# Kernel optimization log

Measured on AMD Instinct MI355X. Metric: run time of the kernel, lower is better.

## Reference

```python
import jax, jax.numpy as jnp
import numpy as np

THETA = 128.0


def _make_Q(d, units):
    # Q[n,m] = (2n+1)/sqrt(d) if n > m and (n+m) odd, else 0 (fixed, non-trainable)
    n = np.arange(d)[:, None]
    m = np.arange(units)[None, :]
    Q = np.where((n > m) & (((n + m) % 2) == 1), (2 * n + 1) / np.sqrt(d), 0.0)
    return jnp.asarray(Q, dtype=jnp.float32)


def setup_inputs() -> dict:
    key = jax.random.key(0)
    k1, k2, k3, k4 = jax.random.split(key, 4)
    B_, T, Din, d, units = 16, 4096, 128, 256, 256
    x = jax.random.normal(k1, (B_, T, Din), dtype=jnp.float32)
    A = jax.random.normal(k2, (d, d), dtype=jnp.float32) / np.sqrt(d)
    Bm = jax.random.normal(k3, (Din, d), dtype=jnp.float32) / np.sqrt(Din)
    W_mix = jax.random.normal(k4, (units, units), dtype=jnp.float32) / np.sqrt(units)
    b_mix = jnp.zeros((units,), dtype=jnp.float32)
    return {"x": x, "A": A, "B": Bm, "W_mix": W_mix, "b_mix": b_mix}


def reference(x, A, B, W_mix, b_mix):
    d = A.shape[0]
    units = W_mix.shape[0]
    Q = _make_Q(d, units)
    QW = Q @ W_mix  # fuse fixed projection with dense kernel: (d, units)
    alpha = 1.0 - 1.0 / THETA
    beta = 1.0 / THETA
    # precompute input projection for all steps: (T, batch, d)
    xB = jnp.einsum('bti,id->tbd', x, B)

    def step(state, xBt):
        new_state = alpha * state + beta * (state @ A + xBt)
        y = jnp.tanh(new_state @ QW + b_mix)
        return new_state, y

    s0 = jnp.zeros((x.shape[0], d), dtype=x.dtype)
    _, ys = jax.lax.scan(step, s0, xB)  # ys: (T, batch, units)
    return jnp.transpose(ys, (1, 0, 2))
```

## Files before the change

kernel.cpp:

```cpp
#include <hip/hip_runtime.h>
#include <math.h>

constexpr int T_   = 4096;
constexpr int NB   = 16;
constexpr int D_   = 256;
constexpr int DIN  = 128;
constexpr int U_   = 256;
constexpr int L1   = 8;
constexpr int C1   = T_ / L1;
constexpr float ALPHA_ = 1.0f - 1.0f / 128.0f;
constexpr float BETA_  = 1.0f / 128.0f;
constexpr int SD   = NB * D_;
constexpr int MS   = D_ * D_;
constexpr int TLP  = D_ + 4;
constexpr int XLP  = DIN + 4;

using short8  = __attribute__((ext_vector_type(8))) short;
using float4v = __attribute__((ext_vector_type(4))) float;

__device__ __forceinline__ unsigned short bf16_rne(float x) {
  const unsigned b = __float_as_uint(x);
  const unsigned r = ((b >> 16) & 1u) + 0x7FFFu;
  return (unsigned short)((b + r) >> 16);
}
__device__ __forceinline__ float bf16_f(unsigned short h) {
  return __uint_as_float(((unsigned)h) << 16);
}

__device__ __forceinline__ void split2(float e0, float e1, unsigned& hd, unsigned& ld) {
  const unsigned b0 = __float_as_uint(e0), b1 = __float_as_uint(e1);
  const unsigned h0 = b0 & 0xFFFF0000u, h1 = b1 & 0xFFFF0000u;
  const float l0 = e0 - __uint_as_float(h0);
  const float l1 = e1 - __uint_as_float(h1);
  hd = (h0 >> 16) | h1;
  ld = (__float_as_uint(l0) >> 16) | (__float_as_uint(l1) & 0xFFFF0000u);
}

__device__ __forceinline__ void unpack8(uint4 a, uint4 b, short8& hi, short8& lo) {
  union { short8 s; unsigned u[4]; } H, L;
  const unsigned d[8] = {a.x, a.y, a.z, a.w, b.x, b.y, b.z, b.w};
#pragma unroll
  for (int i = 0; i < 4; ++i) {
    H.u[i] = (d[2 * i] >> 16) | (d[2 * i + 1] & 0xFFFF0000u);
    L.u[i] = (d[2 * i] & 0xFFFFu) | (d[2 * i + 1] << 16);
  }
  hi = H.s; lo = L.s;
}

__device__ __forceinline__ int nwpar(int c, int l) {
  if (c <= 0) return 0;
  const int f = 31 - __clz(c);
  const int nw = (l < f + 1) ? l : (f + 1);
  return nw & 1;
}

__device__ __forceinline__ void mm_row(const float* __restrict__ Am,
                                       const float* __restrict__ Bm,
                                       float* __restrict__ Dm,
                                       int i, int tid, float* srow) {
  srow[tid] = Am[i * D_ + tid];
  __syncthreads();
  float a0 = 0.f, a1 = 0.f, a2 = 0.f, a3 = 0.f;
#pragma unroll 8
  for (int k = 0; k < D_; k += 4) {
    a0 = fmaf(srow[k + 0], Bm[(k + 0) * D_ + tid], a0);
    a1 = fmaf(srow[k + 1], Bm[(k + 1) * D_ + tid], a1);
    a2 = fmaf(srow[k + 2], Bm[(k + 2) * D_ + tid], a2);
    a3 = fmaf(srow[k + 3], Bm[(k + 3) * D_ + tid], a3);
  }
  Dm[i * D_ + tid] = (a0 + a1) + (a2 + a3);
  __syncthreads();
}

__global__ __launch_bounds__(256) void k_prep(const float* __restrict__ A,
                                              const float* __restrict__ W,
                                              float* __restrict__ Meff,
                                              float* __restrict__ QW,
                                              const float* __restrict__ Bm,
                                              unsigned short* __restrict__ Mf,
                                              unsigned short* __restrict__ Bmf) {
  const int bid = blockIdx.x, tid = threadIdx.x;
  if (bid < D_) {
    float v = BETA_ * A[bid * D_ + tid];
    if (bid == tid) v += ALPHA_;
    Meff[bid * D_ + tid] = v;
    return;
  }
  if (bid == D_) {
    __shared__ float wch[32 * D_];
    float se = 0.f, so = 0.f;
    for (int ch = 0; ch < D_ / 32; ++ch) {
      __syncthreads();
      for (int idx = tid; idx < 32 * D_; idx += 256)
        wch[idx] = W[ch * 32 * D_ + idx];
      __syncthreads();
#pragma unroll
      for (int r = 0; r < 32; ++r) {
        const int n = ch * 32 + r;
        const float sum = (n & 1) ? se : so;
        QW[n * U_ + tid] = sum * ((float)(2 * n + 1) / 16.0f);
        const float wv = wch[r * D_ + tid];
        if (n & 1) so += wv; else se += wv;
      }
    }
    return;
  }
  const int pb = bid - D_ - 1;
  const int lane = tid & 63, nb0 = tid >> 6;
  const int quad = lane >> 4, m16 = lane & 15;
  if (pb < 8) {
    const int ks = pb;
    for (int nb = nb0; nb < 16; nb += 4) {
      const size_t fo = ((size_t)(nb * 8 + ks) * 64 + lane) * 8;
#pragma unroll
      for (int jj = 0; jj < 8; ++jj) {
        const int k = ks * 32 + quad * 8 + jj;
        const int n = nb * 16 + m16;
        const float v = BETA_ * A[k * D_ + n];
        const unsigned short h = bf16_rne(v);
        Mf[fo + jj] = h;
        Mf[MS + fo + jj] = bf16_rne(v - bf16_f(h));
      }
    }
  } else {
    const int ks = pb - 8;
    unsigned short* dh = Bmf;
    unsigned short* dl = Bmf + (MS / 2);
    for (int nb = nb0; nb < 16; nb += 4) {
      const size_t fo = ((size_t)(nb * 4 + ks) * 64 + lane) * 8;
#pragma unroll
      for (int jj = 0; jj < 8; ++jj) {
        const int k = ks * 32 + quad * 8 + jj;
        const int n = nb * 16 + m16;
        const float v = BETA_ * Bm[k * D_ + n];
        const unsigned short h = bf16_rne(v);
        dh[fo + jj] = h;
        dl[fo + jj] = bf16_rne(v - bf16_f(h));
      }
    }
  }
}

__global__ __launch_bounds__(256) void k_pw(const float* __restrict__ Am,
                                            const float* __restrict__ Bbase,
                                            float* __restrict__ Dbase) {
  __shared__ float srow[D_];
  const int q = blockIdx.x >> 8, row = blockIdx.x & 255;
  mm_row(Am, Bbase + (size_t)q * MS, Dbase + (size_t)q * MS, row, threadIdx.x, srow);
}

__global__ __launch_bounds__(256) void k_pwr(const float* __restrict__ Abase,
                                             const float* __restrict__ Bm,
                                             float* __restrict__ Dbase) {
  __shared__ float srow[D_];
  const int q = blockIdx.x >> 8, row = blockIdx.x & 255;
  mm_row(Abase + (size_t)q * MS, Bm, Dbase + (size_t)q * MS, row, threadIdx.x, srow);
}

__global__ __launch_bounds__(256, 2) void k_big2(
    const float* __restrict__ R, const float* __restrict__ QWm,
    const float* __restrict__ M8, unsigned short* __restrict__ Bf,
    unsigned short* __restrict__ Pf0,
    const float* __restrict__ x, const unsigned short* __restrict__ Bmf,
    const unsigned short* __restrict__ Mf,
    unsigned short* __restrict__ Shi, unsigned short* __restrict__ Slo,
    float* __restrict__ Ends) {
  const int bid = blockIdx.x, tid = threadIdx.x;
  if (bid < 80) {
    const int mat = bid >> 3, ks = bid & 7;
    const float* X = (mat < 8) ? (R + (size_t)mat * MS) : (mat == 8 ? QWm : M8);
    unsigned short* dh = (mat < 9) ? (Bf + (size_t)mat * (2 * MS)) : Pf0;
    unsigned short* dl = dh + MS;
    const int lane = tid & 63, nb0 = tid >> 6;
    const int quad = lane >> 4, m16 = lane & 15;
    for (int nb = nb0; nb < 16; nb += 4) {
      const size_t fo = ((size_t)(nb * 8 + ks) * 64 + lane) * 8;
#pragma unroll
      for (int jj = 0; jj < 8; ++jj) {
        const int k = ks * 32 + quad * 8 + jj;
        const int n = nb * 16 + m16;
        const float xv = X[k * D_ + n];
        const unsigned short h = bf16_rne(xv);
        dh[fo + jj] = h;
        dl[fo + jj] = bf16_rne(xv - bf16_f(h));
      }
    }
    return;
  }
  __shared__ __align__(16) float xls[NB][XLP];
  __shared__ __align__(16) unsigned tls[NB][TLP];
  const int c = bid - 80;
  const int w = tid >> 6, lane = tid & 63;
  const int m16 = lane & 15, q = lane >> 4;
  const int xrow = tid >> 4, xi0 = (tid & 15) * 8;

  float4v sC[4];
#pragma unroll
  for (int nt = 0; nt < 4; ++nt) sC[nt] = (float4v){0.f, 0.f, 0.f, 0.f};

  for (int j = 0; j < L1; ++j) {
    const int t = c * L1 + j;
    __syncthreads();
    {
      const float* xr = x + ((size_t)xrow * T_ + t) * DIN + xi0;
      const float4 v0 = *(const float4*)(xr);
      const float4 v1 = *(const float4*)(xr + 4);
      *(float4*)(&xls[xrow][xi0]) = v0;
      *(float4*)(&xls[xrow][xi0 + 4]) = v1;
    }
    if (j > 0) {
#pragma unroll
      for (int nt = 0; nt < 4; ++nt) {
        const int n = (w * 4 + nt) * 16 + m16;
#pragma unroll
        for (int r = 0; r < 4; ++r) {
          const float sv = sC[nt][r];
          const unsigned hb = __float_as_uint(sv) & 0xFFFF0000u;
          const float lo = sv - __uint_as_float(hb);
          tls[4 * q + r][n] = hb | (__float_as_uint(lo) >> 16);
        }
      }
    }
    __syncthreads();
    float4v acc[4];
#pragma unroll
    for (int nt = 0; nt < 4; ++nt) {
      acc[nt][0] = ALPHA_ * sC[nt][0];
      acc[nt][1] = ALPHA_ * sC[nt][1];
      acc[nt][2] = ALPHA_ * sC[nt][2];
      acc[nt][3] = ALPHA_ * sC[nt][3];
    }
#pragma unroll
    for (int ks = 0; ks < 4; ++ks) {
      float xv[8];
      *(float4*)(xv)     = *(const float4*)(&xls[m16][32 * ks + 8 * q]);
      *(float4*)(xv + 4) = *(const float4*)(&xls[m16][32 * ks + 8 * q + 4]);
      union { short8 s; unsigned u[4]; } XH, XL;
#pragma unroll
      for (int p = 0; p < 4; ++p) split2(xv[2 * p], xv[2 * p + 1], XH.u[p], XL.u[p]);
#pragma unroll
      for (int nt = 0; nt < 4; ++nt) {
        const size_t fo = ((size_t)((w * 4 + nt) * 4 + ks) * 64 + lane) * 8;
        const short8 bh = *(const short8*)(Bmf + fo);
        const short8 bl = *(const short8*)(Bmf + (MS / 2) + fo);
        acc[nt] = __builtin_amdgcn_mfma_f32_16x16x32_bf16(XH.s, bh, acc[nt], 0, 0, 0);
        acc[nt] = __builtin_amdgcn_mfma_f32_16x16x32_bf16(XH.s, bl, acc[nt], 0, 0, 0);
        acc[nt] = __builtin_amdgcn_mfma_f32_16x16x32_bf16(XL.s, bh, acc[nt], 0, 0, 0);
      }
    }
    if (j > 0) {
#pragma unroll
      for (int ks = 0; ks < 8; ++ks) {
        const uint4 p0 = *(const uint4*)(&tls[m16][32 * ks + 8 * q]);
        const uint4 p1 = *(const uint4*)(&tls[m16][32 * ks + 8 * q + 4]);
        short8 sh, sl; unpack8(p0, p1, sh, sl);
        if ((ks & 3) == w) {
          const size_t ao = ((size_t)((t - 1) * 8 + ks) * 64 + lane) * 8;
          *(short8*)(Shi + ao) = sh;
          *(short8*)(Slo + ao) = sl;
        }
#pragma unroll
        for (int nt = 0; nt < 4; ++nt) {
          const size_t fo = ((size_t)((w * 4 + nt) * 8 + ks) * 64 + lane) * 8;
          const short8 mh = *(const short8*)(Mf + fo);
          const short8 ml = *(const short8*)(Mf + MS + fo);
          acc[nt] = __builtin_amdgcn_mfma_f32_16x16x32_bf16(sh, mh, acc[nt], 0, 0, 0);
          acc[nt] = __builtin_amdgcn_mfma_f32_16x16x32_bf16(sh, ml, acc[nt], 0, 0, 0);
          acc[nt] = __builtin_amdgcn_mfma_f32_16x16x32_bf16(sl, mh, acc[nt], 0, 0, 0);
        }
      }
    }
#pragma unroll
    for (int nt = 0; nt < 4; ++nt) sC[nt] = acc[nt];
  }
  const int tl = c * L1 + L1 - 1;
  __syncthreads();
#pragma unroll
  for (int nt = 0; nt < 4; ++nt) {
    const int n = (w * 4 + nt) * 16 + m16;
#pragma unroll
    for (int r = 0; r < 4; ++r) {
      const float sv = sC[nt][r];
      const unsigned hb = __float_as_uint(sv) & 0xFFFF0000u;
      const float lo = sv - __uint_as_float(hb);
      tls[4 * q + r][n] = hb | (__float_as_uint(lo) >> 16);
    }
  }
  __syncthreads();
#pragma unroll
  for (int kk = 0; kk < 2; ++kk) {
    const int ks = w + kk * 4;
    const uint4 p0 = *(const uint4*)(&tls[m16][32 * ks + 8 * q]);
    const uint4 p1 = *(const uint4*)(&tls[m16][32 * ks + 8 * q + 4]);
    short8 sh, sl; unpack8(p0, p1, sh, sl);
    const size_t ao = ((size_t)(tl * 8 + ks) * 64 + lane) * 8;
    *(short8*)(Shi + ao) = sh;
    *(short8*)(Slo + ao) = sl;
  }
#pragma unroll
  for (int nt = 0; nt < 4; ++nt) {
    const int n = (w * 4 + nt) * 16 + m16;
#pragma unroll
    for (int r = 0; r < 4; ++r)
      Ends[(size_t)c * SD + (size_t)(4 * q + r) * D_ + n] = sC[nt][r];
  }
}

__global__ __launch_bounds__(256) void k_scan(
    float* V0, float* V1,
    const unsigned short* __restrict__ Pf,
    const float* __restrict__ Pf32,
    float* __restrict__ Psq,
    unsigned short* __restrict__ PfNext,
    int lvl, int do_sq, int packmode,
    unsigned short* __restrict__ Hhi, unsigned short* __restrict__ Hlo) {
  __shared__ __align__(16) float smem[16 * TLP];
  const int bid = blockIdx.x, tid = threadIdx.x;
  const int shift = 1 << lvl;
  const int Cw = packmode ? C1 : (C1 - shift);
  if (bid >= Cw) {
    if (!do_sq) return;
    const int i = bid - Cw;
    smem[tid] = Pf32[i * D_ + tid];
    __syncthreads();
    float a0 = 0.f, a1 = 0.f, a2 = 0.f, a3 = 0.f;
#pragma unroll 8
    for (int k = 0; k < D_; k += 4) {
      a0 = fmaf(smem[k + 0], Pf32[(k + 0) * D_ + tid], a0);
      a1 = fmaf(smem[k + 1], Pf32[(k + 1) * D_ + tid], a1);
      a2 = fmaf(smem[k + 2], Pf32[(k + 2) * D_ + tid], a2);
      a3 = fmaf(smem[k + 3], Pf32[(k + 3) * D_ + tid], a3);
    }
    const float v = (a0 + a1) + (a2 + a3);
    Psq[i * D_ + tid] = v;
    const unsigned short h = bf16_rne(v);
    const unsigned short l = bf16_rne(v - bf16_f(h));
    const size_t off = ((size_t)((tid >> 4) * 8 + (i >> 5)) * 64 +
                        ((i >> 3) & 3) * 16 + (tid & 15)) * 8 + (i & 7);
    PfNext[off] = h;
    PfNext[MS + off] = l;
    return;
  }
  const int c = packmode ? bid : (bid + shift);
  const int w = tid >> 6, lane = tid & 63;
  const int m16 = lane & 15, q = lane >> 4;
  const int ownPar = nwpar(c, lvl);
  const float* Vown = ownPar ? V1 : V0;
  float4v acc[4];
#pragma unroll
  for (int nt = 0; nt < 4; ++nt) {
    const int n = (w * 4 + nt) * 16 + m16;
#pragma unroll
    for (int r = 0; r < 4; ++r)
      acc[nt][r] = Vown[(size_t)c * SD + (size_t)(4 * q + r) * D_ + n];
  }
  if (c >= shift) {
    const float* Vsrc = nwpar(c - shift, lvl) ? V1 : V0;
    const float* src = Vsrc + (size_t)(c - shift) * SD;
    {
      const int row = tid >> 4, col0 = (tid & 15) * 16;
#pragma unroll
      for (int p = 0; p < 4; ++p)
        *(float4*)(&smem[row * TLP + col0 + 4 * p]) =
            *(const float4*)(src + (size_t)row * D_ + col0 + 4 * p);
    }
    __syncthreads();
#pragma unroll
    for (int ks = 0; ks < 8; ++ks) {
      float xv[8];
      *(float4*)(xv)     = *(const float4*)(&smem[m16 * TLP + 32 * ks + 8 * q]);
      *(float4*)(xv + 4) = *(const float4*)(&smem[m16 * TLP + 32 * ks + 8 * q + 4]);
      union { short8 s; unsigned u[4]; } XH, XL;
#pragma unroll
      for (int p = 0; p < 4; ++p) split2(xv[2 * p], xv[2 * p + 1], XH.u[p], XL.u[p]);
#pragma unroll
      for (int nt = 0; nt < 4; ++nt) {
        const size_t fo = ((size_t)((w * 4 + nt) * 8 + ks) * 64 + lane) * 8;
        const short8 ph = *(const short8*)(Pf + fo);
        const short8 pl = *(const short8*)(Pf + MS + fo);
        acc[nt] = __builtin_amdgcn_mfma_f32_16x16x32_bf16(XH.s, ph, acc[nt], 0, 0, 0);
        acc[nt] = __builtin_amdgcn_mfma_f32_16x16x32_bf16(XH.s, pl, acc[nt], 0, 0, 0);
        acc[nt] = __builtin_amdgcn_mfma_f32_16x16x32_bf16(XL.s, ph, acc[nt], 0, 0, 0);
      }
    }
  }
  if (packmode) {
    __syncthreads();
    unsigned* tls = (unsigned*)smem;
#pragma unroll
    for (int nt = 0; nt < 4; ++nt) {
      const int n = (w * 4 + nt) * 16 + m16;
#pragma unroll
      for (int r = 0; r < 4; ++r) {
        const float sv = acc[nt][r];
        const unsigned hb = __float_as_uint(sv) & 0xFFFF0000u;
        const float lo = sv - __uint_as_float(hb);
        tls[(4 * q + r) * TLP + n] = hb | (__float_as_uint(lo) >> 16);
      }
    }
    __syncthreads();
#pragma unroll
    for (int ks = 0; ks < 8; ++ks) {
      const uint4 p0 = *(const uint4*)(&tls[m16 * TLP + 32 * ks + 8 * q]);
      const uint4 p1 = *(const uint4*)(&tls[m16 * TLP + 32 * ks + 8 * q + 4]);
      short8 sh, sl; unpack8(p0, p1, sh, sl);
      const size_t ao = ((size_t)(c * 8 + ks) * 64 + lane) * 8;
      *(short8*)(Hhi + ao) = sh;
      *(short8*)(Hlo + ao) = sl;
    }
  } else {
    float* Vdst = (ownPar ^ 1) ? V1 : V0;
#pragma unroll
    for (int nt = 0; nt < 4; ++nt) {
      const int n = (w * 4 + nt) * 16 + m16;
#pragma unroll
      for (int r = 0; r < 4; ++r)
        Vdst[(size_t)c * SD + (size_t)(4 * q + r) * D_ + n] = acc[nt][r];
    }
  }
}

__global__ __launch_bounds__(256, 3) void k_passB(
    const unsigned short* __restrict__ Shi, const unsigned short* __restrict__ Slo,
    const unsigned short* __restrict__ Hhi, const unsigned short* __restrict__ Hlo,
    const unsigned short* __restrict__ Bf, const float* __restrict__ bmix,
    float* __restrict__ out) {
  const int bid = blockIdx.x;
  const int g4 = (bid >> 3) * 4, j = bid & 7;
  const int tid = threadIdx.x;
  const int w = tid >> 6, lane = tid & 63;
  const int m16 = lane & 15, quad = lane >> 4;
  const unsigned short* Qh = Bf + (size_t)8 * 2 * MS;
  const unsigned short* Ql = Qh + MS;
  const unsigned short* Rh = Bf + (size_t)j * 2 * MS;
  const unsigned short* Rl = Rh + MS;

  float4v acc[4][4];
#pragma unroll
  for (int ci = 0; ci < 4; ++ci)
#pragma unroll
    for (int nt = 0; nt < 4; ++nt) acc[ci][nt] = (float4v){0.f, 0.f, 0.f, 0.f};

  for (int ks = 0; ks < 8; ++ks) {
    short8 fh[4], fl[4];
#pragma unroll
    for (int nt = 0; nt < 4; ++nt) {
      const size_t fo = ((size_t)((w * 4 + nt) * 8 + ks) * 64 + lane) * 8;
      fh[nt] = *(const short8*)(Qh + fo);
      fl[nt] = *(const short8*)(Ql + fo);
    }
#pragma unroll
    for (int ci = 0; ci < 4; ++ci) {
      const int t = (g4 + ci) * 8 + j;
      const size_t ao = ((size_t)(t * 8 + ks) * 64 + lane) * 8;
      const short8 sh = *(const short8*)(Shi + ao);
      const short8 sl = *(const short8*)(Slo + ao);
#pragma unroll
      for (int nt = 0; nt < 4; ++nt) {
        float4v a = acc[ci][nt];
        a = __builtin_amdgcn_mfma_f32_16x16x32_bf16(sh, fh[nt], a, 0, 0, 0);
        a = __builtin_amdgcn_mfma_f32_16x16x32_bf16(sh, fl[nt], a, 0, 0, 0);
        a = __builtin_amdgcn_mfma_f32_16x16x32_bf16(sl, fh[nt], a, 0, 0, 0);
        acc[ci][nt] = a;
      }
    }
#pragma unroll
    for (int nt = 0; nt < 4; ++nt) {
      const size_t fo = ((size_t)((w * 4 + nt) * 8 + ks) * 64 + lane) * 8;
      fh[nt] = *(const short8*)(Rh + fo);
      fl[nt] = *(const short8*)(Rl + fo);
    }
#pragma unroll
    for (int ci = 0; ci < 4; ++ci) {
      const int c = g4 + ci;
      if (c > 0) {
        const size_t ho = ((size_t)((c - 1) * 8 + ks) * 64 + lane) * 8;
        const short8 hh = *(const short8*)(Hhi + ho);
        const short8 hl = *(const short8*)(Hlo + ho);
#pragma unroll
        for (int nt = 0; nt < 4; ++nt) {
          float4v a = acc[ci][nt];
          a = __builtin_amdgcn_mfma_f32_16x16x32_bf16(hh, fh[nt], a, 0, 0, 0);
          a = __builtin_amdgcn_mfma_f32_16x16x32_bf16(hh, fl[nt], a, 0, 0, 0);
          a = __builtin_amdgcn_mfma_f32_16x16x32_bf16(hl, fh[nt], a, 0, 0, 0);
          acc[ci][nt] = a;
        }
      }
    }
  }
  __shared__ float ysm[16][U_ + 4];
  for (int ci = 0; ci < 4; ++ci) {
    const int t = (g4 + ci) * 8 + j;
    __syncthreads();
#pragma unroll
    for (int nt = 0; nt < 4; ++nt) {
      const int n = (w * 4 + nt) * 16 + m16;
      const float bias = bmix[n];
#pragma unroll
      for (int r = 0; r < 4; ++r) {
        const float v = acc[ci][nt][r] + bias;
        const float e = __expf(2.0f * v);
        ysm[quad * 4 + r][n] = 1.0f - 2.0f / (e + 1.0f);
      }
    }
    __syncthreads();
    for (int idx = tid; idx < 16 * (U_ / 4); idx += 256) {
      const int b = idx >> 6, c4 = (idx & 63) * 4;
      const float4 v = make_float4(ysm[b][c4], ysm[b][c4 + 1],
                                   ysm[b][c4 + 2], ysm[b][c4 + 3]);
      *(float4*)(out + ((size_t)b * T_ + t) * U_ + c4) = v;
    }
  }
}

extern "C" void kernel_launch(void* const* d_in, const int* in_sizes, int n_in,
                              void* d_out, int out_size, void* d_ws, size_t ws_size,
                              hipStream_t stream) {
  const float* x    = (const float*)d_in[0];
  const float* A    = (const float*)d_in[1];
  const float* Bm   = (const float*)d_in[2];
  const float* W    = (const float*)d_in[3];
  const float* bmix = (const float*)d_in[4];
  float* out = (float*)d_out;

  float* ws = (float*)d_ws;
  unsigned short* Shi = (unsigned short*)ws;
  unsigned short* Slo = (unsigned short*)(ws + 8388608);
  float* pw  = ws + 16777216;
  float* QW  = pw + 8 * (size_t)MS;
  float* R   = QW + MS;
  float* Sa  = R + 8 * (size_t)MS;
  float* Sb  = Sa + MS;
  unsigned short* Bf  = (unsigned short*)(Sb + MS);
  unsigned short* Mf  = Bf + (size_t)9 * 2 * MS;
  unsigned short* Bmf = Mf + 2 * (size_t)MS;
  unsigned short* Pf0 = Bmf + MS;
  unsigned short* Pf1 = Pf0 + 2 * (size_t)MS;
  (void)in_sizes; (void)n_in; (void)out_size; (void)ws_size;

  float* V0 = out;
  float* V1 = out + (size_t)C1 * SD;

  unsigned short* Hhi = (unsigned short*)d_in[0];
  unsigned short* Hlo = Hhi + (size_t)C1 * 16 * 256;

  k_prep<<<D_ + 13, 256, 0, stream>>>(A, W, pw, QW, Bm, Mf, Bmf);
  k_pw<<<256, 256, 0, stream>>>(pw, pw, pw + MS);
  k_pw<<<512, 256, 0, stream>>>(pw + MS, pw, pw + 2 * (size_t)MS);
  k_pw<<<1024, 256, 0, stream>>>(pw + 3 * (size_t)MS, pw, pw + 4 * (size_t)MS);
  k_pwr<<<2048, 256, 0, stream>>>(pw, QW, R);
  k_big2<<<80 + C1, 256, 0, stream>>>(R, QW, pw + 7 * (size_t)MS, Bf, Pf0,
                                      x, Bmf, Mf, Shi, Slo, V0);

  const float* Pcur = pw + 7 * (size_t)MS;
  float* sqs[2] = {Sa, Sb};
  unsigned short* Pfp[2] = {Pf0, Pf1};
  for (int lvl = 0; lvl < 9; ++lvl) {
    float* Pd = sqs[lvl & 1];
    const int pack = (lvl == 8) ? 1 : 0;
    const int do_sq = (lvl < 8) ? 1 : 0;
    const int grid = pack ? C1 : (C1 - (1 << lvl)) + D_;
    k_scan<<<grid, 256, 0, stream>>>(V0, V1, Pfp[lvl & 1], Pcur, Pd,
                                     Pfp[(lvl + 1) & 1], lvl, do_sq, pack,
                                     Hhi, Hlo);
    Pcur = Pd;
  }

  k_passB<<<1024, 256, 0, stream>>>(Shi, Slo, Hhi, Hlo, Bf, bmix, out);
}
```

Measured before the change: 436.8 us.

## Restructure chunk-state scan as odd/even reduction with half-size inner scan

Replaces the 9-level Hillis-Steele scan over 512 chunk states with an odd/even scheme. A first pass combines each pair of chunks, a Hillis-Steele scan then runs over the 256 odd-indexed chunks, and a final pass fixes up the even chunks. This roughly halves the blocks and matrix-multiply work per level. It adds one launch, needs a third packed-power buffer, and makes the ping-pong buffer parity logic more intricate.

After: 431.1 us. Within noise of the previous version (-1.3%).

```diff
diff --git a/kernel.cpp b/kernel.cpp
--- a/kernel.cpp
+++ b/kernel.cpp
@@ -47,11 +47,11 @@
   hi = H.s; lo = L.s;
 }
 
-__device__ __forceinline__ int nwpar(int c, int l) {
-  if (c <= 0) return 0;
-  const int f = 31 - __clz(c);
-  const int nw = (l < f + 1) ? l : (f + 1);
-  return nw & 1;
+__device__ __forceinline__ int nw_before(int k, int l) {
+  const int nt = (k <= 0) ? 0 : (31 - __clz(k)) + 1;
+  int cap = l - 1; if (cap > 8) cap = 8;
+  const int m = cap < nt ? cap : nt;
+  return 1 + m;
 }
 
 __device__ __forceinline__ void mm_row(const float* __restrict__ Am,
@@ -306,21 +306,23 @@
   }
 }
 
-__global__ __launch_bounds__(256) void k_scan(
+__global__ __launch_bounds__(256) void k_scanO(
     float* V0, float* V1,
     const unsigned short* __restrict__ Pf,
     const float* __restrict__ Pf32,
     float* __restrict__ Psq,
     unsigned short* __restrict__ PfNext,
-    int lvl, int do_sq, int packmode,
+    int do_sq, int phase,
     unsigned short* __restrict__ Hhi, unsigned short* __restrict__ Hlo) {
   __shared__ __align__(16) float smem[16 * TLP];
   const int bid = blockIdx.x, tid = threadIdx.x;
-  const int shift = 1 << lvl;
-  const int Cw = packmode ? C1 : (C1 - shift);
-  if (bid >= Cw) {
+  int Wb;
+  if (phase == 0) Wb = 256;
+  else if (phase < 8) Wb = 256 - (1 << (phase - 1));
+  else Wb = 256;
+  if (bid >= Wb) {
     if (!do_sq) return;
-    const int i = bid - Cw;
+    const int i = bid - Wb;
     smem[tid] = Pf32[i * D_ + tid];
     __syncthreads();
     float a0 = 0.f, a1 = 0.f, a2 = 0.f, a3 = 0.f;
@@ -341,22 +343,53 @@
     PfNext[MS + off] = l;
     return;
   }
-  const int c = packmode ? bid : (bid + shift);
+  int k, c, csrc = 0;
+  const float* ownBuf;
+  const float* srcBuf = nullptr;
+  float* dstBuf = nullptr;
+  bool hasSrc, dofp32, dopack;
+  if (phase == 0) {
+    k = bid; c = 2 * k + 1;
+    ownBuf = V0; srcBuf = V0; csrc = c - 1;
+    dstBuf = V1; hasSrc = true; dofp32 = true; dopack = false;
+  } else if (phase <= 8) {
+    const int s = 1 << (phase - 1);
+    k = (phase < 8) ? (bid + s) : bid;
+    c = 2 * k + 1;
+    const int p0 = nw_before(k, phase) & 1;
+    ownBuf = p0 ? V1 : V0;
+    hasSrc = (k >= s);
+    if (hasSrc) {
+      const int ko = k - s;
+      srcBuf = (nw_before(ko, phase) & 1) ? V1 : V0;
+      csrc = 2 * ko + 1;
+    }
+    dstBuf = (p0 ^ 1) ? V1 : V0;
+    dofp32 = hasSrc;
+    dopack = (phase == 8);
+  } else {
+    k = bid; c = 2 * k;
+    ownBuf = V0;
+    hasSrc = (k >= 1);
+    if (hasSrc) {
+      const int ko = k - 1;
+      srcBuf = (nw_before(ko, 9) & 1) ? V1 : V0;
+      csrc = 2 * ko + 1;
+    }
+    dofp32 = false; dopack = true;
+  }
   const int w = tid >> 6, lane = tid & 63;
   const int m16 = lane & 15, q = lane >> 4;
-  const int ownPar = nwpar(c, lvl);
-  const float* Vown = ownPar ? V1 : V0;
   float4v acc[4];
 #pragma unroll
   for (int nt = 0; nt < 4; ++nt) {
     const int n = (w * 4 + nt) * 16 + m16;
 #pragma unroll
     for (int r = 0; r < 4; ++r)
-      acc[nt][r] = Vown[(size_t)c * SD + (size_t)(4 * q + r) * D_ + n];
-  }
-  if (c >= shift) {
-    const float* Vsrc = nwpar(c - shift, lvl) ? V1 : V0;
-    const float* src = Vsrc + (size_t)(c - shift) * SD;
+      acc[nt][r] = ownBuf[(size_t)c * SD + (size_t)(4 * q + r) * D_ + n];
+  }
+  if (hasSrc) {
+    const float* src = srcBuf + (size_t)csrc * SD;
     {
       const int row = tid >> 4, col0 = (tid & 15) * 16;
 #pragma unroll
@@ -384,7 +417,16 @@
       }
     }
   }
-  if (packmode) {
+  if (dofp32) {
+#pragma unroll
+    for (int nt = 0; nt < 4; ++nt) {
+      const int n = (w * 4 + nt) * 16 + m16;
+#pragma unroll
+      for (int r = 0; r < 4; ++r)
+        dstBuf[(size_t)c * SD + (size_t)(4 * q + r) * D_ + n] = acc[nt][r];
+    }
+  }
+  if (dopack) {
     __syncthreads();
     unsigned* tls = (unsigned*)smem;
 #pragma unroll
@@ -407,15 +449,6 @@
       const size_t ao = ((size_t)(c * 8 + ks) * 64 + lane) * 8;
       *(short8*)(Hhi + ao) = sh;
       *(short8*)(Hlo + ao) = sl;
-    }
-  } else {
-    float* Vdst = (ownPar ^ 1) ? V1 : V0;
-#pragma unroll
-    for (int nt = 0; nt < 4; ++nt) {
-      const int n = (w * 4 + nt) * 16 + m16;
-#pragma unroll
-      for (int r = 0; r < 4; ++r)
-        Vdst[(size_t)c * SD + (size_t)(4 * q + r) * D_ + n] = acc[nt][r];
     }
   }
 }
@@ -536,6 +569,7 @@
   unsigned short* Bmf = Mf + 2 * (size_t)MS;
   unsigned short* Pf0 = Bmf + MS;
   unsigned short* Pf1 = Pf0 + 2 * (size_t)MS;
+  unsigned short* Pf2 = Pf1 + 2 * (size_t)MS;
   (void)in_sizes; (void)n_in; (void)out_size; (void)ws_size;
 
   float* V0 = out;
@@ -552,19 +586,20 @@
   k_big2<<<80 + C1, 256, 0, stream>>>(R, QW, pw + 7 * (size_t)MS, Bf, Pf0,
                                       x, Bmf, Mf, Shi, Slo, V0);
 
-  const float* Pcur = pw + 7 * (size_t)MS;
-  float* sqs[2] = {Sa, Sb};
-  unsigned short* Pfp[2] = {Pf0, Pf1};
-  for (int lvl = 0; lvl < 9; ++lvl) {
-    float* Pd = sqs[lvl & 1];
-    const int pack = (lvl == 8) ? 1 : 0;
-    const int do_sq = (lvl < 8) ? 1 : 0;
-    const int grid = pack ? C1 : (C1 - (1 << lvl)) + D_;
-    k_scan<<<grid, 256, 0, stream>>>(V0, V1, Pfp[lvl & 1], Pcur, Pd,
-                                     Pfp[(lvl + 1) & 1], lvl, do_sq, pack,
-                                     Hhi, Hlo);
-    Pcur = Pd;
-  }
+  float* sqbuf[2] = {Sa, Sb};
+  unsigned short* plbuf[2] = {Pf1, Pf2};
+  k_scanO<<<512, 256, 0, stream>>>(V0, V1, Pf0, pw + 7 * (size_t)MS,
+                                   sqbuf[0], plbuf[0], 1, 0, Hhi, Hlo);
+  for (int p = 1; p <= 7; ++p) {
+    const int Wb = 256 - (1 << (p - 1));
+    k_scanO<<<Wb + 256, 256, 0, stream>>>(V0, V1, plbuf[(p - 1) & 1],
+                                          sqbuf[(p - 1) & 1], sqbuf[p & 1],
+                                          plbuf[p & 1], 1, p, Hhi, Hlo);
+  }
+  k_scanO<<<256, 256, 0, stream>>>(V0, V1, plbuf[1], nullptr, nullptr, nullptr,
+                                   0, 8, Hhi, Hlo);
+  k_scanO<<<256, 256, 0, stream>>>(V0, V1, Pf0, nullptr, nullptr, nullptr,
+                                   0, 9, Hhi, Hlo);
 
   k_passB<<<1024, 256, 0, stream>>>(Shi, Slo, Hhi, Hlo, Bf, bmix, out);
 }
```
